# Kernel tuning notes

Hardware: AMD Instinct MI355X
Metric: run time of the kernel (lower is better)

Reference implementation:

```python
import jax, jax.numpy as jnp
import numpy as np


def setup_inputs() -> dict:
    key = jax.random.key(0)
    k1, k2 = jax.random.split(key)
    completed = jax.random.normal(k1, (8, 8192, 3), dtype=jnp.float32)
    partial = jax.random.normal(k2, (8, 4096, 3), dtype=jnp.float32)
    return {"completed": completed, "partial": partial}


def reference(completed, partial) -> jnp.ndarray:
    # torch.cdist(partial, completed): (B, M, N) pairwise Euclidean distances
    # d^2 = ||p||^2 + ||c||^2 - 2 p.c  (computed via GEMM, matching cdist math)
    p_sq = jnp.sum(partial * partial, axis=-1, keepdims=True)          # (B, M, 1)
    c_sq = jnp.sum(completed * completed, axis=-1, keepdims=True)       # (B, N, 1)
    cross = jnp.einsum("bmd,bnd->bmn", partial, completed)             # (B, M, N)
    d2 = p_sq + jnp.swapaxes(c_sq, 1, 2) - 2.0 * cross                  # (B, M, N)
    dist = jnp.sqrt(jnp.maximum(d2, 0.0))
    min_dist = jnp.min(dist, axis=2)                                    # (B, M)
    return jnp.mean(min_dist)
```

## Files before the change

### kernel.cpp

```cpp
#include <hip/hip_runtime.h>


constexpr int B  = 8;
constexpr int N  = 8192;
constexpr int M  = 4096;
constexpr int NT = 256;
constexpr int TP = 8;
constexpr int MBLK = NT * TP;
constexpr int MC   = M / MBLK;
constexpr int NBLK = 256;
constexpr int NC   = N / NBLK;
constexpr int TOTAL_PM = B * M;

__global__ __launch_bounds__(NT) void pml_main(const float* __restrict__ completed,
                                               const float* __restrict__ partial,
                                               float* __restrict__ ws) {
    __shared__ float4 cs[NBLK];
    const int t     = threadIdx.x;
    const int b     = blockIdx.z;
    const int mBase = blockIdx.y * MBLK;
    const int nBase = blockIdx.x * NBLK;

    {
        const float* cp = completed + (size_t)(b * N + nBase + t) * 3;
        float x = cp[0], y = cp[1], z = cp[2];
        cs[t] = make_float4(x, y, z, 0.5f * (x * x + y * y + z * z));
    }
    __syncthreads();

    const int m0 = mBase + t * TP;
    const float* pp = partial + (size_t)(b * M + m0) * 3;

    float nx[TP], ny[TP], nz[TP], fm[TP];
#pragma unroll
    for (int p = 0; p < TP; ++p) {
        float x = pp[3 * p + 0];
        float y = pp[3 * p + 1];
        float z = pp[3 * p + 2];
        nx[p] = -x; ny[p] = -y; nz[p] = -z;
        fm[p] = 3.402823466e38f;
    }

#pragma unroll 2
    for (int j = 0; j < NBLK; ++j) {
        float4 c = cs[j];
#pragma unroll
        for (int p = 0; p < TP; ++p) {
            float f = fmaf(nx[p], c.x, fmaf(ny[p], c.y, fmaf(nz[p], c.z, c.w)));
            fm[p] = fminf(fm[p], f);
        }
    }

    float o[TP];
#pragma unroll
    for (int p = 0; p < TP; ++p) {
        float x = nx[p], y = ny[p], z = nz[p];
        float psq = x * x + y * y + z * z;
        o[p] = fmaxf(fmaf(2.0f, fm[p], psq), 0.0f);
    }

    float4* wsv = (float4*)(ws + (size_t)blockIdx.x * TOTAL_PM + b * M + m0);
    wsv[0] = make_float4(o[0], o[1], o[2], o[3]);
    wsv[1] = make_float4(o[4], o[5], o[6], o[7]);
}

constexpr int RBLOCKS = 64;
constexpr int RT      = 256;
constexpr int RPT     = TOTAL_PM / (RBLOCKS * RT);

__global__ __launch_bounds__(RT) void pml_reduce(const float* __restrict__ ws,
                                                 float* __restrict__ out) {
    const int gid = blockIdx.x * RT + threadIdx.x;
    float s = 0.0f;
#pragma unroll
    for (int k = 0; k < RPT; ++k) {
        int idx = gid + k * (RBLOCKS * RT);
        float m = 3.402823466e38f;
#pragma unroll
        for (int c = 0; c < NC; ++c)
            m = fminf(m, ws[(size_t)c * TOTAL_PM + idx]);
        s += sqrtf(m);
    }
#pragma unroll
    for (int off = 32; off > 0; off >>= 1) s += __shfl_down(s, off);

    __shared__ float red[RT / 64];
    const int lane = threadIdx.x & 63;
    const int wid  = threadIdx.x >> 6;
    if (lane == 0) red[wid] = s;
    __syncthreads();
    if (threadIdx.x == 0) {
        float tot = red[0] + red[1] + red[2] + red[3];
        atomicAdd(out, tot * (1.0f / (float)TOTAL_PM));
    }
}

__global__ void pml_zero(float* out) { out[0] = 0.0f; }

extern "C" void kernel_launch(void* const* d_in, const int* in_sizes, int n_in,
                              void* d_out, int out_size, void* d_ws, size_t ws_size,
                              hipStream_t stream) {
    const float* completed = (const float*)d_in[0];
    const float* partial   = (const float*)d_in[1];
    float* out = (float*)d_out;
    float* ws  = (float*)d_ws;

    pml_zero<<<1, 1, 0, stream>>>(out);

    dim3 grid(NC, MC, B);
    pml_main<<<grid, NT, 0, stream>>>(completed, partial, ws);

    pml_reduce<<<RBLOCKS, RT, 0, stream>>>(ws, out);
}
```

Measured before the change: 84.62 us.

## Retile distance kernel over full M per block and move finalization into reduce

Each thread now handles 16 partial points and each block covers all of M against a 64-point slice of completed, loaded with vectorized float4 reads. The inner loop processes two completed points per iteration to shorten the min dependency chains. Zeroing the output is folded into the main kernel, removing one launch. The squared-norm and sqrt work moves into the reduce kernel. The cost is a workspace four times larger, which adds global memory traffic, and higher register pressure.

```diff
diff --git a/kernel.cpp b/kernel.cpp
--- a/kernel.cpp
+++ b/kernel.cpp
@@ -5,82 +5,85 @@
 constexpr int N  = 8192;
 constexpr int M  = 4096;
 constexpr int NT = 256;
-constexpr int TP = 8;
-constexpr int MBLK = NT * TP;
-constexpr int MC   = M / MBLK;
-constexpr int NBLK = 256;
+constexpr int TP = 16;
+constexpr int NBLK = 64;
 constexpr int NC   = N / NBLK;
-constexpr int TOTAL_PM = B * M;
+constexpr int ROWS = B * M;
+constexpr float FMAX = 3.402823466e38f;
 
-__global__ __launch_bounds__(NT) void pml_main(const float* __restrict__ completed,
-                                               const float* __restrict__ partial,
-                                               float* __restrict__ ws) {
+__global__ __launch_bounds__(NT, 4) void pml_main(const float* __restrict__ completed,
+                                                  const float* __restrict__ partial,
+                                                  float* __restrict__ ws,
+                                                  float* __restrict__ out) {
     __shared__ float4 cs[NBLK];
     const int t     = threadIdx.x;
-    const int b     = blockIdx.z;
-    const int mBase = blockIdx.y * MBLK;
+    const int b     = blockIdx.y;
     const int nBase = blockIdx.x * NBLK;
 
-    {
+    if (blockIdx.x == 0 && b == 0 && t == 0) out[0] = 0.0f;
+
+    if (t < NBLK) {
         const float* cp = completed + (size_t)(b * N + nBase + t) * 3;
         float x = cp[0], y = cp[1], z = cp[2];
         cs[t] = make_float4(x, y, z, 0.5f * (x * x + y * y + z * z));
     }
     __syncthreads();
 
-    const int m0 = mBase + t * TP;
-    const float* pp = partial + (size_t)(b * M + m0) * 3;
+    const int m0 = t * TP;
+    const float4* pv = (const float4*)(partial + (size_t)(b * M + m0) * 3);
+    float a[3 * TP];
+    float4* av = (float4*)a;
+#pragma unroll
+    for (int i = 0; i < 3 * TP / 4; ++i) av[i] = pv[i];
 
     float nx[TP], ny[TP], nz[TP], fm[TP];
 #pragma unroll
     for (int p = 0; p < TP; ++p) {
-        float x = pp[3 * p + 0];
-        float y = pp[3 * p + 1];
-        float z = pp[3 * p + 2];
-        nx[p] = -x; ny[p] = -y; nz[p] = -z;
-        fm[p] = 3.402823466e38f;
+        nx[p] = -a[3 * p + 0];
+        ny[p] = -a[3 * p + 1];
+        nz[p] = -a[3 * p + 2];
+        fm[p] = FMAX;
     }
 
-#pragma unroll 2
-    for (int j = 0; j < NBLK; ++j) {
-        float4 c = cs[j];
+#pragma unroll 4
+    for (int j = 0; j < NBLK; j += 2) {
+        float4 c0 = cs[j];
+        float4 c1 = cs[j + 1];
 #pragma unroll
         for (int p = 0; p < TP; ++p) {
-            float f = fmaf(nx[p], c.x, fmaf(ny[p], c.y, fmaf(nz[p], c.z, c.w)));
-            fm[p] = fminf(fm[p], f);
+            float f0 = fmaf(nx[p], c0.x, fmaf(ny[p], c0.y, fmaf(nz[p], c0.z, c0.w)));
+            float f1 = fmaf(nx[p], c1.x, fmaf(ny[p], c1.y, fmaf(nz[p], c1.z, c1.w)));
+            fm[p] = fminf(fm[p], fminf(f0, f1));
         }
     }
 
     float o[TP];
 #pragma unroll
-    for (int p = 0; p < TP; ++p) {
-        float x = nx[p], y = ny[p], z = nz[p];
-        float psq = x * x + y * y + z * z;
-        o[p] = fmaxf(fmaf(2.0f, fm[p], psq), 0.0f);
-    }
-
-    float4* wsv = (float4*)(ws + (size_t)blockIdx.x * TOTAL_PM + b * M + m0);
-    wsv[0] = make_float4(o[0], o[1], o[2], o[3]);
-    wsv[1] = make_float4(o[4], o[5], o[6], o[7]);
+    for (int p = 0; p < TP; ++p) o[p] = fm[p];
+    float4* wsv = (float4*)(ws + (size_t)blockIdx.x * ROWS + b * M + m0);
+#pragma unroll
+    for (int i = 0; i < TP / 4; ++i)
+        wsv[i] = make_float4(o[4 * i], o[4 * i + 1], o[4 * i + 2], o[4 * i + 3]);
 }
 
-constexpr int RBLOCKS = 64;
-constexpr int RT      = 256;
-constexpr int RPT     = TOTAL_PM / (RBLOCKS * RT);
+constexpr int RT = 256;
+constexpr int RBLOCKS = ROWS / RT;
 
 __global__ __launch_bounds__(RT) void pml_reduce(const float* __restrict__ ws,
+                                                 const float* __restrict__ partial,
                                                  float* __restrict__ out) {
-    const int gid = blockIdx.x * RT + threadIdx.x;
-    float s = 0.0f;
-#pragma unroll
-    for (int k = 0; k < RPT; ++k) {
-        int idx = gid + k * (RBLOCKS * RT);
-        float m = 3.402823466e38f;
-#pragma unroll
-        for (int c = 0; c < NC; ++c)
-            m = fminf(m, ws[(size_t)c * TOTAL_PM + idx]);
-        s += sqrtf(m);
-    }
+    const int row = blockIdx.x * RT + threadIdx.x;
+    float m = FMAX;
+#pragma unroll 8
+    for (int c = 0; c < NC; ++c)
+        m = fminf(m, ws[(size_t)c * ROWS + row]);
+
+    const float* pp = partial + (size_t)row * 3;
+    float x = pp[0], y = pp[1], z = pp[2];
+    float psq = x * x + y * y + z * z;
+    float d2  = fmaxf(fmaf(2.0f, m, psq), 0.0f);
+    float s   = sqrtf(d2);
+
 #pragma unroll
     for (int off = 32; off > 0; off >>= 1) s += __shfl_down(s, off);
 
@@ -91,11 +94,9 @@
     __syncthreads();
     if (threadIdx.x == 0) {
         float tot = red[0] + red[1] + red[2] + red[3];
-        atomicAdd(out, tot * (1.0f / (float)TOTAL_PM));
+        atomicAdd(out, tot * (1.0f / (float)ROWS));
     }
 }
-
-__global__ void pml_zero(float* out) { out[0] = 0.0f; }
 
 extern "C" void kernel_launch(void* const* d_in, const int* in_sizes, int n_in,
                               void* d_out, int out_size, void* d_ws, size_t ws_size,
@@ -105,10 +106,7 @@
     float* out = (float*)d_out;
     float* ws  = (float*)d_ws;
 
-    pml_zero<<<1, 1, 0, stream>>>(out);
-
-    dim3 grid(NC, MC, B);
-    pml_main<<<grid, NT, 0, stream>>>(completed, partial, ws);
-
-    pml_reduce<<<RBLOCKS, RT, 0, stream>>>(ws, out);
+    dim3 grid(NC, B);
+    pml_main<<<grid, NT, 0, stream>>>(completed, partial, ws, out);
+    pml_reduce<<<RBLOCKS, RT, 0, stream>>>(ws, partial, out);
 }
```

New measurement: 99.90 us. 1.18x slower.
